# Performance work log

Measured on AMD Instinct MI355X. Metric: run time of the kernel, lower is better.

The kernel has to match this reference:

```python
import jax, jax.numpy as jnp
import numpy as np

NUM_HEADS = 16
NUM_KV_HEADS = 4
HEAD_DIM = 128
BASE_THETA = 10000.0


def _rope_cos_sin(seq_len, head_dim, dtype):
    # standard (ntk_alpha=1) rotate-half RoPE tables: [S, head_dim]
    inv_freq = 1.0 / (BASE_THETA ** (jnp.arange(0, head_dim, 2, dtype=jnp.float32) / head_dim))
    angles = jnp.arange(seq_len, dtype=jnp.float32)[:, None] * inv_freq[None, :]  # [S, D/2]
    cos = jnp.concatenate([jnp.cos(angles), jnp.cos(angles)], axis=-1).astype(dtype)
    sin = jnp.concatenate([jnp.sin(angles), jnp.sin(angles)], axis=-1).astype(dtype)
    return cos, sin


def _rotate_half(t):
    half = t.shape[-1] // 2
    return jnp.concatenate([-t[..., half:], t[..., :half]], axis=-1)


def setup_inputs() -> dict:
    key = jax.random.key(0)
    ks = jax.random.split(key, 5)
    B, S, E = 2, 2048, 2048
    KV = NUM_KV_HEADS * HEAD_DIM  # 512
    scale = 0.02
    return {
        "x": jax.random.normal(ks[0], (B, S, E), dtype=jnp.float32),
        "Wq": jax.random.normal(ks[1], (E, E), dtype=jnp.float32) * scale,
        "Wk": jax.random.normal(ks[2], (E, KV), dtype=jnp.float32) * scale,
        "Wv": jax.random.normal(ks[3], (E, KV), dtype=jnp.float32) * scale,
        "Wo": jax.random.normal(ks[4], (E, E), dtype=jnp.float32) * scale,
    }


def reference(x, Wq, Wk, Wv, Wo):
    B, S, E = x.shape
    n_rep = NUM_HEADS // NUM_KV_HEADS
    scale = 1.0 / jnp.sqrt(jnp.float32(HEAD_DIM))

    # QKV projections (bias=False)
    q = (x @ Wq).reshape(B, S, NUM_HEADS, HEAD_DIM)
    k = (x @ Wk).reshape(B, S, NUM_KV_HEADS, HEAD_DIM)
    v = (x @ Wv).reshape(B, S, NUM_KV_HEADS, HEAD_DIM)

    # dynamic RoPE on q, k
    cos, sin = _rope_cos_sin(S, HEAD_DIM, x.dtype)
    cos = cos[None, :, None, :]
    sin = sin[None, :, None, :]
    q = q * cos + _rotate_half(q) * sin
    k = k * cos + _rotate_half(k) * sin

    # GQA: repeat kv heads to match query heads
    k = jnp.repeat(k, n_rep, axis=2)
    v = jnp.repeat(v, n_rep, axis=2)

    # [B, H, S, D]
    q = q.transpose(0, 2, 1, 3)
    k = k.transpose(0, 2, 1, 3)
    v = v.transpose(0, 2, 1, 3)

    # causal mask (window_size=0 -> standard causal, additive float mask)
    i = jnp.arange(S)[:, None]
    j = jnp.arange(S)[None, :]
    neg = jnp.finfo(jnp.float32).min
    causal = jnp.where(j > i, neg, 0.0).astype(jnp.float32)  # [S, S]

    scores = jnp.einsum("bhqd,bhkd->bhqk", q, k) * scale
    scores = scores + causal[None, None, :, :]
    weights = jax.nn.softmax(scores.astype(jnp.float32), axis=-1)
    attn = jnp.einsum("bhqk,bhkd->bhqd", weights.astype(v.dtype), v)

    attn = attn.transpose(0, 2, 1, 3).reshape(B, S, E)
    return attn @ Wo
```

## Files before the change

kernel.cpp:

```cpp
#include <hip/hip_runtime.h>
#include <math.h>


typedef __attribute__((ext_vector_type(8))) short short8;
typedef __attribute__((ext_vector_type(4))) float f32x4;
typedef __attribute__((ext_vector_type(16))) float f32x16;

typedef const __attribute__((address_space(1))) void* gvp;
typedef __attribute__((address_space(3))) void* svp;

__device__ __forceinline__ void async16(const void* g, void* l) {
  __builtin_amdgcn_global_load_lds((gvp)g, (svp)l, 16, 0, 0);
}
__device__ __forceinline__ void wait_vm0() { asm volatile("s_waitcnt vmcnt(0)" ::: "memory"); }
__device__ __forceinline__ void wait_vm4() { asm volatile("s_waitcnt vmcnt(4)" ::: "memory"); }
__device__ __forceinline__ void wait_vm8() { asm volatile("s_waitcnt vmcnt(8)" ::: "memory"); }
__device__ __forceinline__ void barrier_raw() { asm volatile("s_barrier" ::: "memory"); }

__device__ __forceinline__ unsigned short f2b(float f) {
  unsigned int u = __builtin_bit_cast(unsigned int, f);
  u += 0x7fffu + ((u >> 16) & 1u);
  return (unsigned short)(u >> 16);
}
__device__ __forceinline__ float b2f(unsigned short h) {
  unsigned int u = ((unsigned int)h) << 16;
  return __builtin_bit_cast(float, u);
}

__device__ __forceinline__ unsigned int pk_bf16(float a, float b) {
  unsigned int r;
  asm("v_cvt_pk_bf16_f32 %0, %1, %2" : "=v"(r) : "v"(a), "v"(b));
  return r;
}
__device__ __forceinline__ void plswap(unsigned int& a, unsigned int& b) {
  asm("v_permlane32_swap_b32 %0, %1" : "+v"(a), "+v"(b));
}

__global__ __launch_bounds__(256) void prep(const float* __restrict__ x,
                                            const float* __restrict__ Wq,
                                            const float* __restrict__ Wk,
                                            const float* __restrict__ Wv,
                                            const float* __restrict__ Wo,
                                            unsigned short* __restrict__ xb,
                                            unsigned short* __restrict__ WqkvT,
                                            unsigned short* __restrict__ WoT) {
  __shared__ float t[32][33];
  if (blockIdx.x < 4096) {
    int i = blockIdx.x * 256 + threadIdx.x;
    const float4* p = (const float4*)x + (size_t)i * 2;
    float4 a = p[0], b4 = p[1];
    union { short8 v; unsigned short u[8]; } o;
    o.u[0] = f2b(a.x);  o.u[1] = f2b(a.y);  o.u[2] = f2b(a.z);  o.u[3] = f2b(a.w);
    o.u[4] = f2b(b4.x); o.u[5] = f2b(b4.y); o.u[6] = f2b(b4.z); o.u[7] = f2b(b4.w);
    ((short8*)xb)[i] = o.v;
    return;
  }
  int idx = blockIdx.x - 4096;
  const float* W; unsigned short* WT; int N, tx, ty;
  const int K = 2048;
  if (idx < 4096)      { W = Wq; WT = WqkvT;                         N = 2048; idx -= 0;    tx = idx & 63; ty = idx >> 6; }
  else if (idx < 5120) { W = Wk; WT = WqkvT + (size_t)2048 * 2048;   N = 512;  idx -= 4096; tx = idx & 15; ty = idx >> 4; }
  else if (idx < 6144) { W = Wv; WT = WqkvT + (size_t)2560 * 2048;   N = 512;  idx -= 5120; tx = idx & 15; ty = idx >> 4; }
  else                 { W = Wo; WT = WoT;                           N = 2048; idx -= 6144; tx = idx & 63; ty = idx >> 6; }
  int c = threadIdx.x & 31, r0 = threadIdx.x >> 5;
  int k0 = ty * 32, n0 = tx * 32;
#pragma unroll
  for (int r = r0; r < 32; r += 8) t[r][c] = W[(size_t)(k0 + r) * N + n0 + c];
  __syncthreads();
#pragma unroll
  for (int r = r0; r < 32; r += 8) WT[(size_t)(n0 + r) * K + k0 + c] = f2b(t[c][r]);
}

#define GQ_STAGE(J, BUF)                                                      \
  { int kb_ = (J) * 32;                                                       \
    _Pragma("unroll") for (int i = 0; i < 2; ++i) {                           \
      int row = w * 32 + i * 16 + (lane >> 2);                                \
      int gc = (lane & 3) ^ (row & 3);                                        \
      async16(Ab + (size_t)row * K + kb_ + gc * 8,                            \
              &As[BUF][(w * 32 + i * 16) * 32]);                              \
      async16(Bb + (size_t)row * K + kb_ + gc * 8,                            \
              &Bs[BUF][(w * 32 + i * 16) * 32]); } }

#define GQ_COMPUTE(CUR)                                                       \
  { const unsigned short* as_ = &As[CUR][0];                                  \
    const unsigned short* bs_ = &Bs[CUR][0];                                  \
    short8 af[4], bfv[4];                                                     \
    _Pragma("unroll") for (int mi = 0; mi < 4; ++mi) {                        \
      int row = wm * 64 + mi * 16 + l15;                                      \
      af[mi] = *(const short8*)&as_[row * 32 + ((quad ^ (row & 3)) * 8)]; }   \
    _Pragma("unroll") for (int ni = 0; ni < 4; ++ni) {                        \
      int row = wn * 64 + ni * 16 + l15;                                      \
      bfv[ni] = *(const short8*)&bs_[row * 32 + ((quad ^ (row & 3)) * 8)]; }  \
    _Pragma("unroll") for (int mi = 0; mi < 4; ++mi)                          \
      _Pragma("unroll") for (int ni = 0; ni < 4; ++ni)                        \
        acc[mi][ni] = __builtin_amdgcn_mfma_f32_16x16x32_bf16(                \
            af[mi], bfv[ni], acc[mi][ni], 0, 0, 0); }

#define GQ_LOOP                                                               \
  GQ_STAGE(0, 0); GQ_STAGE(1, 1); GQ_STAGE(2, 2);                             \
  const int nIter = K >> 5;                                                   \
  for (int j = 0; j < nIter; ++j) {                                           \
    if (j + 2 < nIter) wait_vm8();                                            \
    else if (j + 1 < nIter) wait_vm4();                                       \
    else wait_vm0();                                                          \
    barrier_raw();                                                            \
    if (j + 3 < nIter) GQ_STAGE(j + 3, (j + 3) & 3);                          \
    GQ_COMPUTE(j & 3);                                                        \
  }

__global__ __launch_bounds__(256) void gemm_bt(const unsigned short* __restrict__ A,
                                               const unsigned short* __restrict__ BT,
                                               void* __restrict__ Cout,
                                               int M, int N, int K, int out_bf16) {
  const int n0 = blockIdx.x * 128;
  const int m0 = blockIdx.y * 128;
  const int tid = threadIdx.x;
  const int w = tid >> 6, lane = tid & 63, l15 = lane & 15, quad = lane >> 4;
  const int wm = w >> 1, wn = w & 1;

  __shared__ __align__(16) unsigned short As[4][128 * 32];
  __shared__ __align__(16) unsigned short Bs[4][128 * 32];

  f32x4 acc[4][4];
#pragma unroll
  for (int mi = 0; mi < 4; mi++)
#pragma unroll
    for (int ni = 0; ni < 4; ni++) acc[mi][ni] = (f32x4){0.f, 0.f, 0.f, 0.f};

  const unsigned short* Ab = A + (size_t)m0 * K;
  const unsigned short* Bb = BT + (size_t)n0 * K;

  GQ_LOOP

  if (out_bf16) {
    unsigned short* C = (unsigned short*)Cout;
#pragma unroll
    for (int mi = 0; mi < 4; mi++)
#pragma unroll
      for (int ni = 0; ni < 4; ni++)
#pragma unroll
        for (int r = 0; r < 4; r++) {
          int row = m0 + wm * 64 + mi * 16 + quad * 4 + r;
          int col = n0 + wn * 64 + ni * 16 + l15;
          C[(size_t)row * N + col] = f2b(acc[mi][ni][r]);
        }
  } else {
    float* C = (float*)Cout;
#pragma unroll
    for (int mi = 0; mi < 4; mi++)
#pragma unroll
      for (int ni = 0; ni < 4; ni++)
#pragma unroll
        for (int r = 0; r < 4; r++) {
          int row = m0 + wm * 64 + mi * 16 + quad * 4 + r;
          int col = n0 + wn * 64 + ni * 16 + l15;
          C[(size_t)row * N + col] = acc[mi][ni][r];
        }
  }
}

#define SC_TOT 0.12753785056274918f
__global__ __launch_bounds__(256) void gemm_qkv(const unsigned short* __restrict__ A,
                                                const unsigned short* __restrict__ BT,
                                                unsigned short* __restrict__ Qm,
                                                unsigned short* __restrict__ Km,
                                                unsigned short* __restrict__ Vtm) {
  const int K = 2048;
  const int n0 = blockIdx.x * 128;
  const int m0 = blockIdx.y * 128;
  const int tid = threadIdx.x;
  const int w = tid >> 6, lane = tid & 63, l15 = lane & 15, quad = lane >> 4;
  const int wm = w >> 1, wn = w & 1;

  __shared__ __align__(16) unsigned char smem[65536];
  unsigned short (*As)[128 * 32] = (unsigned short (*)[128 * 32])smem;
  unsigned short (*Bs)[128 * 32] = (unsigned short (*)[128 * 32])(smem + 32768);
  float* L = (float*)smem;

  f32x4 acc[4][4];
#pragma unroll
  for (int mi = 0; mi < 4; mi++)
#pragma unroll
    for (int ni = 0; ni < 4; ni++) acc[mi][ni] = (f32x4){0.f, 0.f, 0.f, 0.f};

  const unsigned short* Ab = A + (size_t)m0 * K;
  const unsigned short* Bb = BT + (size_t)n0 * K;

  GQ_LOOP

  __syncthreads();
#pragma unroll
  for (int mi = 0; mi < 4; mi++)
#pragma unroll
    for (int ni = 0; ni < 4; ni++)
#pragma unroll
      for (int r = 0; r < 4; r++) {
        int rr = wm * 64 + mi * 16 + quad * 4 + r;
        int cc = wn * 64 + ni * 16 + l15;
        L[rr * 128 + (cc ^ (rr & 31))] = acc[mi][ni][r];
      }
  __syncthreads();

  const int head = blockIdx.x;
  const int b = m0 >> 11;
  const int s_base = m0 & 2047;

  if (head < 20) {
    const int d = tid & 63, sl = tid >> 6;
    const bool isQ = head < 16;
    unsigned short* dq = isQ
      ? Qm + ((size_t)((b * 16 + head) * 2048 + s_base)) * 128
      : Km + ((size_t)((b * 4 + (head - 16)) * 2048 + s_base)) * 128;
    const float invf = exp2f(-0.20762050593046f * (float)d);
#pragma unroll 4
    for (int i = 0; i < 32; i++) {
      int s = sl + i * 4;
      float lo = b2f(f2b(L[s * 128 + (d ^ (s & 31))]));
      float hi = b2f(f2b(L[s * 128 + ((d + 64) ^ (s & 31))]));
      float ang = (float)(s_base + s) * invf;
      float sn, cs;
      sincosf(ang, &sn, &cs);
      float nlo = lo * cs - hi * sn;
      float nhi = hi * cs + lo * sn;
      if (isQ) { nlo *= SC_TOT; nhi *= SC_TOT; }
      dq[(size_t)s * 128 + d]      = f2b(nlo);
      dq[(size_t)s * 128 + d + 64] = f2b(nhi);
    }
  } else {
    const int kv = head - 20;
    const int s_l = tid & 63, dl = tid >> 6;
    unsigned short* dv = Vtm + ((size_t)(b * 4 + kv) * 128) * 2048;
#pragma unroll 2
    for (int sh = 0; sh < 2; sh++) {
      int s = sh * 64 + s_l;
#pragma unroll 4
      for (int i = 0; i < 32; i++) {
        int d = i * 4 + dl;
        dv[(size_t)d * 2048 + s_base + s] = f2b(L[s * 128 + (d ^ (s & 31))]);
      }
    }
  }
}

#define FIXED_M 12.0f

__device__ __forceinline__ void proc_acc(const f32x16& s, bool msk, int kvb, int q,
                                         float& l_own, short8& paL, short8& paH) {
  float p[16];
#pragma unroll
  for (int r = 0; r < 16; r++) {
    float v = exp2f(s[r] - FIXED_M);
    if (msk) {
      int kv = kvb + (r & 3) + 8 * (r >> 2);
      if (kv > q) v = 0.f;
    }
    p[r] = v;
    l_own += v;
  }
  unsigned int u0 = pk_bf16(p[0], p[1]),  u1 = pk_bf16(p[2], p[3]);
  unsigned int u2 = pk_bf16(p[4], p[5]),  u3 = pk_bf16(p[6], p[7]);
  plswap(u0, u2); plswap(u1, u3);
  unsigned int w0 = pk_bf16(p[8], p[9]),  w1 = pk_bf16(p[10], p[11]);
  unsigned int w2 = pk_bf16(p[12], p[13]), w3 = pk_bf16(p[14], p[15]);
  plswap(w0, w2); plswap(w1, w3);
  union { unsigned int u[4]; short8 s8; } a, b;
  a.u[0] = u0; a.u[1] = u1; a.u[2] = u2; a.u[3] = u3;
  b.u[0] = w0; b.u[1] = w1; b.u[2] = w2; b.u[3] = w3;
  paL = a.s8; paH = b.s8;
}

__global__ __launch_bounds__(512, 2) void flash2(const unsigned short* __restrict__ Q,
                                                 const unsigned short* __restrict__ Kc,
                                                 const unsigned short* __restrict__ Vt,
                                                 unsigned short* __restrict__ attn) {
  const int pair = blockIdx.x;
  const int h = blockIdx.y;
  const int b = blockIdx.z;
  const int kvh = h >> 2;
  const int tid = threadIdx.x;
  const int w = tid >> 6;
  const int g = w >> 2;
  const int wg = w & 3;
  const int lane = tid & 63;
  const int l31 = lane & 31, hi = lane >> 5, x7 = l31 & 7;

  __shared__ __align__(16) unsigned short kbuf[2][2][64 * 128];
  __shared__ __align__(16) unsigned short vbuf[2][2][128 * 64];
  __shared__ float lx[2][4][32];
  __shared__ float li[2][4][32];

  const unsigned short* Qb = Q  + ((size_t)(b * 16 + h)) * 2048 * 128;
  const unsigned short* Kb = Kc + ((size_t)(b * 4 + kvh)) * 2048 * 128;
  const unsigned short* Vb = Vt + ((size_t)(b * 4 + kvh)) * 128 * 2048;

  for (int t = 0; t < 2; t++) {
    const int qt = (t == 0) ? pair : (15 - pair);
    const int q0 = qt * 128;
    const int qw = q0 + wg * 32;
    const int qv = qw + l31;
    const int half = qt + 1;
    const int j0 = g * half;

    short8 qf[8];
    {
      const unsigned short* qp = Qb + (size_t)qv * 128 + hi * 8;
#pragma unroll
      for (int s = 0; s < 8; s++) qf[s] = *(const short8*)(qp + s * 16);
    }

    f32x16 o[4];
#pragma unroll
    for (int d = 0; d < 4; d++)
#pragma unroll
      for (int e = 0; e < 16; e++) o[d][e] = 0.f;
    float l_own = 0.f;

    __syncthreads();

#pragma unroll
    for (int k2 = 0; k2 < 4; k2++) {
      int m = wg * 4 + k2;
      int rl = m * 4 + (lane >> 4);
      int c8 = (lane & 15) ^ (rl & 7);
      async16(Kb + (size_t)(j0 * 64 + rl) * 128 + c8 * 8, &kbuf[g][0][m * 512]);
    }
#pragma unroll
    for (int k2 = 0; k2 < 4; k2++) {
      int m = wg * 4 + k2;
      int d = m * 8 + (lane >> 3);
      int c3 = (lane & 7) ^ (d & 7);
      async16(Vb + (size_t)d * 2048 + j0 * 64 + c3 * 8, &vbuf[g][0][m * 512]);
    }

    for (int i = 0; i < half; i++) {
      wait_vm0();
      barrier_raw();
      const int cur = i & 1;
      const int kb = (j0 + i) * 64;

      if (i + 1 < half) {
        int kb2 = kb + 64;
#pragma unroll
        for (int k2 = 0; k2 < 4; k2++) {
          int m = wg * 4 + k2;
          int rl = m * 4 + (lane >> 4);
          int c8 = (lane & 15) ^ (rl & 7);
          async16(Kb + (size_t)(kb2 + rl) * 128 + c8 * 8, &kbuf[g][cur ^ 1][m * 512]);
        }
#pragma unroll
        for (int k2 = 0; k2 < 4; k2++) {
          int m = wg * 4 + k2;
          int d = m * 8 + (lane >> 3);
          int c3 = (lane & 7) ^ (d & 7);
          async16(Vb + (size_t)d * 2048 + kb2 + c3 * 8, &vbuf[g][cur ^ 1][m * 512]);
        }
      }

      if (kb <= qw + 31) {
        f32x16 sA, sB;
#pragma unroll
        for (int e = 0; e < 16; e++) { sA[e] = 0.f; sB[e] = 0.f; }
        const unsigned short* kp = &kbuf[g][cur][0];
        __builtin_amdgcn_s_setprio(1);
#pragma unroll
        for (int s = 0; s < 8; s++) {
          int ch = (((s << 1) | hi) ^ x7) << 3;
          short8 ka = *(const short8*)&kp[l31 * 128 + ch];
          short8 kB2 = *(const short8*)&kp[(32 + l31) * 128 + ch];
          sA = __builtin_amdgcn_mfma_f32_32x32x16_bf16(ka, qf[s], sA, 0, 0, 0);
          sB = __builtin_amdgcn_mfma_f32_32x32x16_bf16(kB2, qf[s], sB, 0, 0, 0);
        }
        __builtin_amdgcn_s_setprio(0);

        const bool msk = (kb + 63 > qw);
        short8 pa[4];
        proc_acc(sA, msk, kb + 4 * hi, qv, l_own, pa[0], pa[1]);
        proc_acc(sB, msk, kb + 32 + 4 * hi, qv, l_own, pa[2], pa[3]);

        const unsigned short* vp = &vbuf[g][cur][0];
        __builtin_amdgcn_s_setprio(1);
#pragma unroll
        for (int db = 0; db < 4; db++) {
          int ro = (db * 32 + l31) * 64;
#pragma unroll
          for (int f = 0; f < 4; f++) {
            int ch = (((f << 1) | hi) ^ x7) << 3;
            short8 vf = *(const short8*)&vp[ro + ch];
            o[db] = __builtin_amdgcn_mfma_f32_32x32x16_bf16(pa[f], vf, o[db], 0, 0, 0);
          }
        }
        __builtin_amdgcn_s_setprio(0);
      }
    }

    __syncthreads();
    {
      float* wout = (float*)&kbuf[g ^ 1][0][0];
      float lown = l_own + __shfl_xor(l_own, 32);
      if (hi == 0) lx[g][wg][l31] = lown;
      const int base = wg * 2048 + lane * 4;
      if (g == 0) {
#pragma unroll
        for (int r4 = 0; r4 < 4; r4++) {
          *(f32x4*)&wout[base + 0 * 1024 + r4 * 256] =
            (f32x4){ o[2][r4 * 4 + 0], o[2][r4 * 4 + 1], o[2][r4 * 4 + 2], o[2][r4 * 4 + 3] };
          *(f32x4*)&wout[base + 1 * 1024 + r4 * 256] =
            (f32x4){ o[3][r4 * 4 + 0], o[3][r4 * 4 + 1], o[3][r4 * 4 + 2], o[3][r4 * 4 + 3] };
        }
      } else {
#pragma unroll
        for (int r4 = 0; r4 < 4; r4++) {
          *(f32x4*)&wout[base + 0 * 1024 + r4 * 256] =
            (f32x4){ o[0][r4 * 4 + 0], o[0][r4 * 4 + 1], o[0][r4 * 4 + 2], o[0][r4 * 4 + 3] };
          *(f32x4*)&wout[base + 1 * 1024 + r4 * 256] =
            (f32x4){ o[1][r4 * 4 + 0], o[1][r4 * 4 + 1], o[1][r4 * 4 + 2], o[1][r4 * 4 + 3] };
        }
      }
      __syncthreads();
      const float* rin = (const float*)&kbuf[g][0][0];
      float ltot = lown + lx[g ^ 1][wg][l31];
      if (hi == 0) li[g][wg][l31] = 1.f / ltot;
      f32x4 inv4[4];
#pragma unroll
      for (int tt = 0; tt < 4; tt++) inv4[tt] = *(const f32x4*)&li[g][wg][tt * 8 + 4 * hi];

      unsigned short* ap0 = attn + ((size_t)(b * 2048 + qw)) * 2048 + h * 128 + l31;
      if (g == 0) {
#pragma unroll
        for (int r4 = 0; r4 < 4; r4++) {
          f32x4 v0 = *(const f32x4*)&rin[base + 0 * 1024 + r4 * 256];
          f32x4 v1 = *(const f32x4*)&rin[base + 1 * 1024 + r4 * 256];
#pragma unroll
          for (int k = 0; k < 4; k++) {
            o[0][r4 * 4 + k] += v0[k];
            o[1][r4 * 4 + k] += v1[k];
          }
        }
#pragma unroll
        for (int r = 0; r < 16; r++) {
          int rowq = (r & 3) + 8 * (r >> 2) + 4 * hi;
          float iv = inv4[r >> 2][r & 3];
          ap0[(size_t)rowq * 2048 + 0]  = f2b(o[0][r] * iv);
          ap0[(size_t)rowq * 2048 + 32] = f2b(o[1][r] * iv);
        }
      } else {
#pragma unroll
        for (int r4 = 0; r4 < 4; r4++) {
          f32x4 v0 = *(const f32x4*)&rin[base + 0 * 1024 + r4 * 256];
          f32x4 v1 = *(const f32x4*)&rin[base + 1 * 1024 + r4 * 256];
#pragma unroll
          for (int k = 0; k < 4; k++) {
            o[2][r4 * 4 + k] += v0[k];
            o[3][r4 * 4 + k] += v1[k];
          }
        }
#pragma unroll
        for (int r = 0; r < 16; r++) {
          int rowq = (r & 3) + 8 * (r >> 2) + 4 * hi;
          float iv = inv4[r >> 2][r & 3];
          ap0[(size_t)rowq * 2048 + 64] = f2b(o[2][r] * iv);
          ap0[(size_t)rowq * 2048 + 96] = f2b(o[3][r] * iv);
        }
      }
    }
  }
}

extern "C" void kernel_launch(void* const* d_in, const int* in_sizes, int n_in,
                              void* d_out, int out_size, void* d_ws, size_t ws_size,
                              hipStream_t stream) {
  const float* x  = (const float*)d_in[0];
  const float* Wq = (const float*)d_in[1];
  const float* Wk = (const float*)d_in[2];
  const float* Wv = (const float*)d_in[3];
  const float* Wo = (const float*)d_in[4];
  float* out = (float*)d_out;

  char* ws = (char*)d_ws;
  unsigned short* xb    = (unsigned short*)(ws);
  unsigned short* WqkvT = (unsigned short*)(ws + 16777216);
  unsigned short* WoT   = (unsigned short*)(ws + 29360128);
  unsigned short* Qm    = (unsigned short*)(ws + 62914560);
  unsigned short* Km    = (unsigned short*)(ws + 79691776);
  unsigned short* Vtm   = (unsigned short*)(ws + 83886080);
  unsigned short* attn  = xb;

  prep<<<14336, 256, 0, stream>>>(x, Wq, Wk, Wv, Wo, xb, WqkvT, WoT);

  gemm_qkv<<<dim3(24, 32), 256, 0, stream>>>(xb, WqkvT, Qm, Km, Vtm);

  flash2<<<dim3(8, 16, 2), 512, 0, stream>>>(Qm, Km, Vtm, attn);

  gemm_bt<<<dim3(16, 32), 256, 0, stream>>>(attn, WoT, out, 4096, 2048, 2048, 0);
}
```

Before: 308.2 us.

## Cut GEMM LDS to three stages and bf16 epilogue for 3 blocks/CU

Shrinks the GEMM software pipeline from four LDS buffers (prefetch depth 3) to three (prefetch depth 2), which lowers shared memory from 64KB to 48KB per block. Both GEMM kernels also get a launch-bounds minimum of 3 blocks per CU. The QKV epilogue now stages bf16 values with a padded row stride of 130 instead of fp32 with an XOR swizzle, so it fits in the smaller buffer. The LDS swizzle changes to use bits 1-2 of the row. The aim is more latency hiding through occupancy, at the cost of a shallower prefetch and possible register pressure from the launch-bounds cap.

```diff
diff --git a/kernel.cpp b/kernel.cpp
--- a/kernel.cpp
+++ b/kernel.cpp
@@ -14,7 +14,6 @@
 }
 __device__ __forceinline__ void wait_vm0() { asm volatile("s_waitcnt vmcnt(0)" ::: "memory"); }
 __device__ __forceinline__ void wait_vm4() { asm volatile("s_waitcnt vmcnt(4)" ::: "memory"); }
-__device__ __forceinline__ void wait_vm8() { asm volatile("s_waitcnt vmcnt(8)" ::: "memory"); }
 __device__ __forceinline__ void barrier_raw() { asm volatile("s_barrier" ::: "memory"); }
 
 __device__ __forceinline__ unsigned short f2b(float f) {
@@ -75,7 +74,7 @@
   { int kb_ = (J) * 32;                                                       \
     _Pragma("unroll") for (int i = 0; i < 2; ++i) {                           \
       int row = w * 32 + i * 16 + (lane >> 2);                                \
-      int gc = (lane & 3) ^ (row & 3);                                        \
+      int gc = (lane & 3) ^ ((row >> 1) & 3);                                 \
       async16(Ab + (size_t)row * K + kb_ + gc * 8,                            \
               &As[BUF][(w * 32 + i * 16) * 32]);                              \
       async16(Bb + (size_t)row * K + kb_ + gc * 8,                            \
@@ -87,39 +86,40 @@
     short8 af[4], bfv[4];                                                     \
     _Pragma("unroll") for (int mi = 0; mi < 4; ++mi) {                        \
       int row = wm * 64 + mi * 16 + l15;                                      \
-      af[mi] = *(const short8*)&as_[row * 32 + ((quad ^ (row & 3)) * 8)]; }   \
+      af[mi] = *(const short8*)&as_[row * 32 + ((quad ^ ((row >> 1) & 3)) * 8)]; } \
     _Pragma("unroll") for (int ni = 0; ni < 4; ++ni) {                        \
       int row = wn * 64 + ni * 16 + l15;                                      \
-      bfv[ni] = *(const short8*)&bs_[row * 32 + ((quad ^ (row & 3)) * 8)]; }  \
+      bfv[ni] = *(const short8*)&bs_[row * 32 + ((quad ^ ((row >> 1) & 3)) * 8)]; } \
     _Pragma("unroll") for (int mi = 0; mi < 4; ++mi)                          \
       _Pragma("unroll") for (int ni = 0; ni < 4; ++ni)                        \
         acc[mi][ni] = __builtin_amdgcn_mfma_f32_16x16x32_bf16(                \
             af[mi], bfv[ni], acc[mi][ni], 0, 0, 0); }
 
 #define GQ_LOOP                                                               \
-  GQ_STAGE(0, 0); GQ_STAGE(1, 1); GQ_STAGE(2, 2);                             \
+  GQ_STAGE(0, 0); GQ_STAGE(1, 1);                                             \
   const int nIter = K >> 5;                                                   \
-  for (int j = 0; j < nIter; ++j) {                                           \
-    if (j + 2 < nIter) wait_vm8();                                            \
-    else if (j + 1 < nIter) wait_vm4();                                       \
-    else wait_vm0();                                                          \
-    barrier_raw();                                                            \
-    if (j + 3 < nIter) GQ_STAGE(j + 3, (j + 3) & 3);                          \
-    GQ_COMPUTE(j & 3);                                                        \
-  }
-
-__global__ __launch_bounds__(256) void gemm_bt(const unsigned short* __restrict__ A,
-                                               const unsigned short* __restrict__ BT,
-                                               void* __restrict__ Cout,
-                                               int M, int N, int K, int out_bf16) {
+  { int c3 = 0, s3 = 2;                                                       \
+    for (int j = 0; j < nIter; ++j) {                                         \
+      if (j + 1 < nIter) wait_vm4(); else wait_vm0();                         \
+      barrier_raw();                                                          \
+      if (j + 2 < nIter) GQ_STAGE(j + 2, s3);                                 \
+      GQ_COMPUTE(c3);                                                         \
+      c3 = (c3 == 2) ? 0 : c3 + 1;                                            \
+      s3 = (s3 == 2) ? 0 : s3 + 1;                                            \
+    } }
+
+__global__ __launch_bounds__(256, 3) void gemm_bt(const unsigned short* __restrict__ A,
+                                                  const unsigned short* __restrict__ BT,
+                                                  void* __restrict__ Cout,
+                                                  int M, int N, int K, int out_bf16) {
   const int n0 = blockIdx.x * 128;
   const int m0 = blockIdx.y * 128;
   const int tid = threadIdx.x;
   const int w = tid >> 6, lane = tid & 63, l15 = lane & 15, quad = lane >> 4;
   const int wm = w >> 1, wn = w & 1;
 
-  __shared__ __align__(16) unsigned short As[4][128 * 32];
-  __shared__ __align__(16) unsigned short Bs[4][128 * 32];
+  __shared__ __align__(16) unsigned short As[3][128 * 32];
+  __shared__ __align__(16) unsigned short Bs[3][128 * 32];
 
   f32x4 acc[4][4];
 #pragma unroll
@@ -160,11 +160,11 @@
 }
 
 #define SC_TOT 0.12753785056274918f
-__global__ __launch_bounds__(256) void gemm_qkv(const unsigned short* __restrict__ A,
-                                                const unsigned short* __restrict__ BT,
-                                                unsigned short* __restrict__ Qm,
-                                                unsigned short* __restrict__ Km,
-                                                unsigned short* __restrict__ Vtm) {
+__global__ __launch_bounds__(256, 3) void gemm_qkv(const unsigned short* __restrict__ A,
+                                                   const unsigned short* __restrict__ BT,
+                                                   unsigned short* __restrict__ Qm,
+                                                   unsigned short* __restrict__ Km,
+                                                   unsigned short* __restrict__ Vtm) {
   const int K = 2048;
   const int n0 = blockIdx.x * 128;
   const int m0 = blockIdx.y * 128;
@@ -172,10 +172,10 @@
   const int w = tid >> 6, lane = tid & 63, l15 = lane & 15, quad = lane >> 4;
   const int wm = w >> 1, wn = w & 1;
 
-  __shared__ __align__(16) unsigned char smem[65536];
+  __shared__ __align__(16) unsigned char smem[49152];
   unsigned short (*As)[128 * 32] = (unsigned short (*)[128 * 32])smem;
-  unsigned short (*Bs)[128 * 32] = (unsigned short (*)[128 * 32])(smem + 32768);
-  float* L = (float*)smem;
+  unsigned short (*Bs)[128 * 32] = (unsigned short (*)[128 * 32])(smem + 24576);
+  unsigned short* L = (unsigned short*)smem;
 
   f32x4 acc[4][4];
 #pragma unroll
@@ -197,7 +197,7 @@
       for (int r = 0; r < 4; r++) {
         int rr = wm * 64 + mi * 16 + quad * 4 + r;
         int cc = wn * 64 + ni * 16 + l15;
-        L[rr * 128 + (cc ^ (rr & 31))] = acc[mi][ni][r];
+        L[rr * 130 + cc] = f2b(acc[mi][ni][r]);
       }
   __syncthreads();
 
@@ -215,8 +215,8 @@
 #pragma unroll 4
     for (int i = 0; i < 32; i++) {
       int s = sl + i * 4;
-      float lo = b2f(f2b(L[s * 128 + (d ^ (s & 31))]));
-      float hi = b2f(f2b(L[s * 128 + ((d + 64) ^ (s & 31))]));
+      float lo = b2f(L[s * 130 + d]);
+      float hi = b2f(L[s * 130 + d + 64]);
       float ang = (float)(s_base + s) * invf;
       float sn, cs;
       sincosf(ang, &sn, &cs);
@@ -236,7 +236,7 @@
 #pragma unroll 4
       for (int i = 0; i < 32; i++) {
         int d = i * 4 + dl;
-        dv[(size_t)d * 2048 + s_base + s] = f2b(L[s * 128 + (d ^ (s & 31))]);
+        dv[(size_t)d * 2048 + s_base + s] = L[s * 130 + d];
       }
     }
   }
```

Result: faster. 295.6 us (-4.1%).
